# Optimization experiments

Hardware: AMD Instinct MI355X
Metric: run time of the kernel (lower is better)

The kernel has to match this reference:

```python
import jax, jax.numpy as jnp
import numpy as np

K = 7          # kernel_size
PAD = K // 2   # padding


def _unfold(t):
    """im2col for kxk neighborhood: (B,C,H,W) -> (B,C,K*K,H,W), zero-padded."""
    B, C, H, W = t.shape
    p = jnp.pad(t, ((0, 0), (0, 0), (PAD, PAD), (PAD, PAD)))
    # row-major over kernel offsets matches F.unfold ordering
    wins = jnp.stack([p[:, :, i:i + H, j:j + W]
                      for i in range(K) for j in range(K)], axis=2)
    return wins


def setup_inputs() -> dict:
    key = jax.random.key(0)
    ks = jax.random.split(key, 7)
    B, C, H, W = 8, 128, 64, 64
    scale = 1.0 / np.sqrt(C)
    x = jax.random.normal(ks[0], (B, C, H, W), dtype=jnp.float32)
    Wq = jax.random.normal(ks[1], (C, C), dtype=jnp.float32) * scale
    Wk = jax.random.normal(ks[2], (C, C), dtype=jnp.float32) * scale
    Wv = jax.random.normal(ks[3], (C, C), dtype=jnp.float32) * scale
    bq = jax.random.normal(ks[4], (C,), dtype=jnp.float32) * 0.01
    bk = jax.random.normal(ks[5], (C,), dtype=jnp.float32) * 0.01
    bv = jax.random.normal(ks[6], (C,), dtype=jnp.float32) * 0.01
    return {"x": x, "Wq": Wq, "bq": bq, "Wk": Wk, "bk": bk, "Wv": Wv, "bv": bv}


def reference(x, Wq, bq, Wk, bk, Wv, bv):
    # 1x1 convs = channel GEMMs
    q = jnp.einsum('oc,bchw->bohw', Wq, x) + bq[:, None, None]
    k = jnp.einsum('oc,bchw->bohw', Wk, x) + bk[:, None, None]
    v = jnp.einsum('oc,bchw->bohw', Wv, x) + bv[:, None, None]
    k_unf = _unfold(k)   # (B,C,K*K,H,W)
    v_unf = _unfold(v)   # (B,C,K*K,H,W)
    # attention scores over the K*K neighborhood, summed over channels
    attn = jnp.einsum('bchw,bcphw->bphw', q, k_unf)
    attn = jax.nn.softmax(attn, axis=1)
    y = jnp.einsum('bphw,bcphw->bchw', attn, v_unf)
    return y
```

## Files before the change

### kernel.cpp

```cpp
#include <hip/hip_runtime.h>
#include <hip/hip_bf16.h>

#define CC   128
#define HH_  64
#define WW_  64
#define BB   8
#define HWSZ (HH_*WW_)
#define CHW  (CC*HWSZ)
#define BCHW (BB*CHW)
#define PAD  3
#define NP   49

typedef __attribute__((ext_vector_type(8))) short short8;
typedef __attribute__((ext_vector_type(4))) float float4v;

__global__ __launch_bounds__(256) void prep_w(
    const float* __restrict__ Wq, const float* __restrict__ Wk,
    const float* __restrict__ Wv,
    unsigned short* __restrict__ whi, unsigned short* __restrict__ wlo)
{
    int i = blockIdx.x * 256 + threadIdx.x;
    const float* src = (i < 16384) ? Wq : (i < 32768 ? Wk : Wv);
    float f = src[i & 16383];
    __hip_bfloat16 h = __float2bfloat16(f);
    float hf = __bfloat162float(h);
    __hip_bfloat16 l = __float2bfloat16(f - hf);
    unsigned short hu, lu;
    __builtin_memcpy(&hu, &h, 2);
    __builtin_memcpy(&lu, &l, 2);
    whi[i] = hu;
    wlo[i] = lu;
}

__global__ __launch_bounds__(256, 2) void qkv_mfma(
    const float* __restrict__ x,
    const unsigned short* __restrict__ whi, const unsigned short* __restrict__ wlo,
    const float* __restrict__ bq, const float* __restrict__ bk,
    const float* __restrict__ bv, float* __restrict__ qkv)
{
    __shared__ unsigned short xT[2][128][136];
    const int proj = blockIdx.y;
    const int n0g  = blockIdx.x << 7;
    const int b    = n0g >> 12;
    const int npx  = n0g & 4095;
    const int tid  = threadIdx.x;
    const int lane = tid & 63;
    const int wv   = tid >> 6;
    const int wm   = wv & 1, wn = wv >> 1;

    const float* xb = x + (size_t)b*CHW + npx;
    #pragma unroll
    for (int it = 0; it < 16; ++it) {
        int f  = tid + (it << 8);
        int c  = f >> 5;
        int p4 = (f & 31) << 2;
        float4 v = *(const float4*)&xb[(size_t)c*HWSZ + p4];
        float vv[4] = {v.x, v.y, v.z, v.w};
        #pragma unroll
        for (int u = 0; u < 4; ++u) {
            __hip_bfloat16 h = __float2bfloat16(vv[u]);
            float hf = __bfloat162float(h);
            __hip_bfloat16 l = __float2bfloat16(vv[u] - hf);
            unsigned short hu, lu;
            __builtin_memcpy(&hu, &h, 2);
            __builtin_memcpy(&lu, &l, 2);
            xT[0][p4 + u][c] = hu;
            xT[1][p4 + u][c] = lu;
        }
    }

    const float* Bp = (proj == 0) ? bq : (proj == 1 ? bk : bv);
    const int q4 = lane >> 4;
    float4v acc[4][4];
    #pragma unroll
    for (int sm = 0; sm < 4; ++sm) {
        const int mb = wm*64 + sm*16 + q4*4;
        float4v bi;
        bi[0] = Bp[mb+0]; bi[1] = Bp[mb+1]; bi[2] = Bp[mb+2]; bi[3] = Bp[mb+3];
        #pragma unroll
        for (int sn = 0; sn < 4; ++sn) acc[sm][sn] = bi;
    }

    __syncthreads();

    const unsigned short* Wh = whi + (size_t)proj*16384;
    const unsigned short* Wl = wlo + (size_t)proj*16384;
    const int kq8  = q4 << 3;
    const int mrow = lane & 15;

    for (int pass = 0; pass < 3; ++pass) {
        const unsigned short* Wp = (pass == 2) ? Wl : Wh;
        const int xi = (pass == 1) ? 1 : 0;
        #pragma unroll
        for (int kc = 0; kc < 4; ++kc) {
            const int kb = kc << 5;
            short8 a[4], bf[4];
            #pragma unroll
            for (int sm = 0; sm < 4; ++sm) {
                const int m = wm*64 + sm*16 + mrow;
                a[sm] = *(const short8*)&Wp[(size_t)m*CC + kb + kq8];
            }
            #pragma unroll
            for (int sn = 0; sn < 4; ++sn) {
                const int n = wn*64 + sn*16 + mrow;
                bf[sn] = *(const short8*)&xT[xi][n][kb + kq8];
            }
            #pragma unroll
            for (int sm = 0; sm < 4; ++sm)
                #pragma unroll
                for (int sn = 0; sn < 4; ++sn)
                    acc[sm][sn] = __builtin_amdgcn_mfma_f32_16x16x32_bf16(
                        a[sm], bf[sn], acc[sm][sn], 0, 0, 0);
        }
    }

    float* op = qkv + (size_t)proj*BCHW + (size_t)b*CHW + npx;
    #pragma unroll
    for (int sm = 0; sm < 4; ++sm) {
        const int mb = wm*64 + sm*16 + q4*4;
        #pragma unroll
        for (int sn = 0; sn < 4; ++sn) {
            const int n = wn*64 + sn*16 + mrow;
            #pragma unroll
            for (int r = 0; r < 4; ++r)
                op[(size_t)(mb + r)*HWSZ + n] = acc[sm][sn][r];
        }
    }
}

__device__ __forceinline__ void load_chunk16(const float* __restrict__ src,
                                             int h0, int c0, float4* stg) {
    const int tid = threadIdx.x;
    #pragma unroll
    for (int i = 0; i < 2; ++i) {
        int f   = tid + (i << 10);
        int c   = f >> 7;
        int rem = f & 127;
        int r   = rem >> 4;
        int q4  = (rem & 15) << 2;
        int hh  = h0 - PAD + r;
        if ((unsigned)hh < (unsigned)HH_)
            stg[i] = *(const float4*)&src[(size_t)(c0 + c)*HWSZ + hh*WW_ + q4];
        else
            stg[i] = make_float4(0.f, 0.f, 0.f, 0.f);
    }
}

__global__ __launch_bounds__(1024) void locatt(
    const float* __restrict__ qkv, float* __restrict__ out)
{
    __shared__ __align__(16) float smem[8*72*17];
    __shared__ float lg[2][NP][64];
    __shared__ float dn[2][64];

    const int blk = blockIdx.x;
    const int xs  = blk & 7;
    const int jj  = blk >> 3;
    const int b   = jj >> 2;
    const int h0  = (((xs << 2) | (jj & 3)) << 1);
    const int tid = threadIdx.x;
    const int s   = tid >> 6;
    const int lane = tid & 63;
    const int q16  = lane & 15;
    const int csub = lane >> 4;
    const int w4   = q16 << 2;
    const int w    = lane;
    const int rsel = s >> 3;
    const int kr   = s & 7;

    const float* qp = qkv + (size_t)b*CHW;
    const float* kp = qkv + (size_t)BCHW + (size_t)b*CHW;
    const float* vp = qkv + (size_t)2*BCHW + (size_t)b*CHW;

    float (*ks)[8][72] = (float(*)[8][72])smem;

    if (tid < 256) {
        int idx = tid & 127;
        int c = idx >> 3, r = idx & 7;
        int col = (tid < 128) ? 0 : 68;
        *(float4*)&ks[c][r][col] = make_float4(0.f, 0.f, 0.f, 0.f);
    }

    const bool active = rsel ? (kr >= 1) : (kr < 7);

    float acc[7][4];
    #pragma unroll
    for (int dx = 0; dx < 7; ++dx)
        #pragma unroll
        for (int j = 0; j < 4; ++j) acc[dx][j] = 0.f;

    float4 stg[2];
    load_chunk16(kp, h0, 0, stg);

    for (int ck = 0; ck < 8; ++ck) {
        #pragma unroll
        for (int i = 0; i < 2; ++i) {
            int f   = tid + (i << 10);
            int c   = f >> 7;
            int rem = f & 127;
            int r   = rem >> 4;
            int q4  = (rem & 15) << 2;
            *(float4*)&ks[c][r][4 + q4] = stg[i];
        }
        __syncthreads();
        if (ck < 7) load_chunk16(kp, h0, (ck + 1) * 16, stg);

        if (active) {
            const int c0 = ck << 4;
            #pragma unroll
            for (int ci4 = 0; ci4 < 4; ++ci4) {
                const int c = (ci4 << 2) + csub;
                const float* qc = qp + (size_t)(c0 + c)*HWSZ
                                     + (size_t)(h0 + rsel)*WW_ + w4;
                float4 qv  = *(const float4*)qc;
                float4 ka  = *(const float4*)&ks[c][kr][w4];
                float4 kb  = *(const float4*)&ks[c][kr][w4 + 4];
                float4 kc2 = *(const float4*)&ks[c][kr][w4 + 8];
                float kw[12] = {ka.x,ka.y,ka.z,ka.w, kb.x,kb.y,kb.z,kb.w,
                                kc2.x,kc2.y,kc2.z,kc2.w};
                float qa[4] = {qv.x,qv.y,qv.z,qv.w};
                #pragma unroll
                for (int dx = 0; dx < 7; ++dx)
                    #pragma unroll
                    for (int j = 0; j < 4; ++j) {
                        float kv = kw[j + dx + 1];
                        acc[dx][j] = fmaf(qa[j], kv, acc[dx][j]);
                    }
            }
        }
        __syncthreads();
    }

    if (active) {
        #pragma unroll
        for (int dx = 0; dx < 7; ++dx)
            #pragma unroll
            for (int j = 0; j < 4; ++j) {
                acc[dx][j] += __shfl_xor(acc[dx][j], 16, 64);
                acc[dx][j] += __shfl_xor(acc[dx][j], 32, 64);
            }
        const int p0 = rsel ? (kr - 1) * 7 : kr * 7;
        #pragma unroll
        for (int dx = 0; dx < 7; ++dx) {
            if ((dx & 3) == csub)
                *(float4*)&lg[rsel][p0 + dx][w4] =
                    make_float4(acc[dx][0], acc[dx][1], acc[dx][2], acc[dx][3]);
        }
    }

    const int cpl   = (s & 7) << 1;
    const int rbase = rsel << 2;
    float vreg[8];
    {
        #pragma unroll
        for (int i = 0; i < 8; ++i) {
            int ch = i >> 2;
            int r  = rbase + (i & 3);
            int hh = h0 - PAD + r;
            vreg[i] = ((unsigned)hh < (unsigned)HH_)
                      ? vp[(size_t)(cpl + ch)*HWSZ + hh*WW_ + w] : 0.f;
        }
    }
    __syncthreads();

    if (tid < 128) {
        const int r = tid >> 6, px = tid & 63;
        float tv[NP];
        float m = -1e30f;
        #pragma unroll
        for (int p = 0; p < NP; ++p) { tv[p] = lg[r][p][px]; m = fmaxf(m, tv[p]); }
        float d = 0.f;
        #pragma unroll
        for (int p = 0; p < NP; ++p) {
            float e = __expf(tv[p] - m);
            d += e;
            lg[r][p][px] = e;
        }
        dn[r][px] = 1.f / d;
    } else {
        int t = tid - 128;
        for (int i = t; i < 1024; i += 896) {
            int r    = i >> 7;
            int rem  = i & 127;
            int colg = rem >> 4;
            int col  = (colg < 4) ? colg : (64 + colg);
            smem[r*1224 + col*17 + (rem & 15)] = 0.f;
        }
    }
    __syncthreads();

    float a[NP];
    const float sc = dn[rsel][w];
    #pragma unroll
    for (int p = 0; p < NP; ++p) a[p] = lg[rsel][p][w] * sc;

    for (int ck = 0; ck < 8; ++ck) {
        #pragma unroll
        for (int i = 0; i < 8; ++i) {
            int ch = i >> 2;
            int r  = rbase + (i & 3);
            smem[r*1224 + (4 + w)*17 + cpl + ch] = vreg[i];
        }
        __syncthreads();
        if (ck < 7) {
            int c0v = (ck + 1) << 4;
            #pragma unroll
            for (int i = 0; i < 8; ++i) {
                int ch = i >> 2;
                int r  = rbase + (i & 3);
                int hh = h0 - PAD + r;
                vreg[i] = ((unsigned)hh < (unsigned)HH_)
                          ? vp[(size_t)(c0v + cpl + ch)*HWSZ + hh*WW_ + w] : 0.f;
            }
        }
        float ya = 0.f, yb = 0.f;
        #pragma unroll
        for (int rl = 0; rl < 7; ++rl) {
            const int r = rl + rsel;
            const float* vbase = &smem[r*1224 + (1 + w)*17 + cpl];
            #pragma unroll
            for (int dx = 0; dx < 7; ++dx) {
                float va = vbase[17*dx];
                float vb = vbase[17*dx + 1];
                float aw = a[rl*7 + dx];
                ya = fmaf(aw, va, ya);
                yb = fmaf(aw, vb, yb);
            }
        }
        float* op = out + (size_t)b*CHW + (size_t)(ck*16 + cpl)*HWSZ
                        + (size_t)(h0 + rsel)*WW_ + w;
        op[0]    = ya;
        op[HWSZ] = yb;
        __syncthreads();
    }
}

extern "C" void kernel_launch(void* const* d_in, const int* in_sizes, int n_in,
                              void* d_out, int out_size, void* d_ws, size_t ws_size,
                              hipStream_t stream) {
    const float* x  = (const float*)d_in[0];
    const float* Wq = (const float*)d_in[1];
    const float* bq = (const float*)d_in[2];
    const float* Wk = (const float*)d_in[3];
    const float* bk = (const float*)d_in[4];
    const float* Wv = (const float*)d_in[5];
    const float* bv = (const float*)d_in[6];
    float* out = (float*)d_out;
    float* qkv = (float*)d_ws;

    unsigned short* whi = (unsigned short*)d_out;
    unsigned short* wlo = whi + 3*16384;

    prep_w  <<<192, 256, 0, stream>>>(Wq, Wk, Wv, whi, wlo);
    qkv_mfma<<<dim3(256, 3), 256, 0, stream>>>(x, whi, wlo, bq, bk, bv, qkv);
    locatt  <<<256, 1024, 0, stream>>>(qkv, out);
}
```

Measured before the change: 149.8 us.

## Split local attention blocks to one output row per 512-thread block

The local-attention kernel now gives each block a single output row with 512 threads, launching 512 blocks instead of 256 blocks of 1024 threads that handled two rows. Each warp covers one kernel row in the score phase and two channels across all 7 neighbor rows in the value phase. Launch bounds request 4 blocks per CU, aiming for more blocks in flight and better latency hiding. The cost is that halo K/V rows are now loaded per single row (7 rows for 1 output instead of 8 for 2), roughly doubling K/V reads, and one of the eight warps sits idle during the score phase.

```diff
diff --git a/kernel.cpp b/kernel.cpp
--- a/kernel.cpp
+++ b/kernel.cpp
@@ -128,45 +128,43 @@
     }
 }
 
-__device__ __forceinline__ void load_chunk16(const float* __restrict__ src,
-                                             int h0, int c0, float4* stg) {
+__device__ __forceinline__ void load_chunk7(const float* __restrict__ src,
+                                            int h, int c0, float4* stg) {
     const int tid = threadIdx.x;
     #pragma unroll
-    for (int i = 0; i < 2; ++i) {
-        int f   = tid + (i << 10);
+    for (int i = 0; i < 4; ++i) {
+        int f   = tid + (i << 9);
         int c   = f >> 7;
         int rem = f & 127;
         int r   = rem >> 4;
         int q4  = (rem & 15) << 2;
-        int hh  = h0 - PAD + r;
-        if ((unsigned)hh < (unsigned)HH_)
+        int hh  = h - PAD + r;
+        if (r < 7 && (unsigned)hh < (unsigned)HH_)
             stg[i] = *(const float4*)&src[(size_t)(c0 + c)*HWSZ + hh*WW_ + q4];
         else
             stg[i] = make_float4(0.f, 0.f, 0.f, 0.f);
     }
 }
 
-__global__ __launch_bounds__(1024) void locatt(
+__global__ __launch_bounds__(512, 4) void locatt(
     const float* __restrict__ qkv, float* __restrict__ out)
 {
-    __shared__ __align__(16) float smem[8*72*17];
-    __shared__ float lg[2][NP][64];
-    __shared__ float dn[2][64];
+    __shared__ __align__(16) float smem[16*8*72];
+    __shared__ float lg[NP][64];
+    __shared__ float dn[64];
 
     const int blk = blockIdx.x;
     const int xs  = blk & 7;
     const int jj  = blk >> 3;
-    const int b   = jj >> 2;
-    const int h0  = (((xs << 2) | (jj & 3)) << 1);
+    const int b   = jj >> 3;
+    const int h   = (xs << 3) | (jj & 7);
     const int tid = threadIdx.x;
-    const int s   = tid >> 6;
+    const int s    = tid >> 6;
     const int lane = tid & 63;
     const int q16  = lane & 15;
     const int csub = lane >> 4;
     const int w4   = q16 << 2;
     const int w    = lane;
-    const int rsel = s >> 3;
-    const int kr   = s & 7;
 
     const float* qp = qkv + (size_t)b*CHW;
     const float* kp = qkv + (size_t)BCHW + (size_t)b*CHW;
@@ -181,7 +179,7 @@
         *(float4*)&ks[c][r][col] = make_float4(0.f, 0.f, 0.f, 0.f);
     }
 
-    const bool active = rsel ? (kr >= 1) : (kr < 7);
+    const bool activeA = (s < 7);
 
     float acc[7][4];
     #pragma unroll
@@ -189,13 +187,13 @@
         #pragma unroll
         for (int j = 0; j < 4; ++j) acc[dx][j] = 0.f;
 
-    float4 stg[2];
-    load_chunk16(kp, h0, 0, stg);
+    float4 stg[4];
+    load_chunk7(kp, h, 0, stg);
 
     for (int ck = 0; ck < 8; ++ck) {
         #pragma unroll
-        for (int i = 0; i < 2; ++i) {
-            int f   = tid + (i << 10);
+        for (int i = 0; i < 4; ++i) {
+            int f   = tid + (i << 9);
             int c   = f >> 7;
             int rem = f & 127;
             int r   = rem >> 4;
@@ -203,19 +201,19 @@
             *(float4*)&ks[c][r][4 + q4] = stg[i];
         }
         __syncthreads();
-        if (ck < 7) load_chunk16(kp, h0, (ck + 1) * 16, stg);
-
-        if (active) {
+        if (ck < 7) load_chunk7(kp, h, (ck + 1) * 16, stg);
+
+        if (activeA) {
             const int c0 = ck << 4;
             #pragma unroll
             for (int ci4 = 0; ci4 < 4; ++ci4) {
                 const int c = (ci4 << 2) + csub;
                 const float* qc = qp + (size_t)(c0 + c)*HWSZ
-                                     + (size_t)(h0 + rsel)*WW_ + w4;
+                                     + (size_t)h*WW_ + w4;
                 float4 qv  = *(const float4*)qc;
-                float4 ka  = *(const float4*)&ks[c][kr][w4];
-                float4 kb  = *(const float4*)&ks[c][kr][w4 + 4];
-                float4 kc2 = *(const float4*)&ks[c][kr][w4 + 8];
+                float4 ka  = *(const float4*)&ks[c][s][w4];
+                float4 kb  = *(const float4*)&ks[c][s][w4 + 4];
+                float4 kc2 = *(const float4*)&ks[c][s][w4 + 8];
                 float kw[12] = {ka.x,ka.y,ka.z,ka.w, kb.x,kb.y,kb.z,kb.w,
                                 kc2.x,kc2.y,kc2.z,kc2.w};
                 float qa[4] = {qv.x,qv.y,qv.z,qv.w};
@@ -231,7 +229,7 @@
         __syncthreads();
     }
 
-    if (active) {
+    if (activeA) {
         #pragma unroll
         for (int dx = 0; dx < 7; ++dx)
             #pragma unroll
@@ -239,47 +237,46 @@
                 acc[dx][j] += __shfl_xor(acc[dx][j], 16, 64);
                 acc[dx][j] += __shfl_xor(acc[dx][j], 32, 64);
             }
-        const int p0 = rsel ? (kr - 1) * 7 : kr * 7;
+        const int p0 = s * 7;
         #pragma unroll
         for (int dx = 0; dx < 7; ++dx) {
             if ((dx & 3) == csub)
-                *(float4*)&lg[rsel][p0 + dx][w4] =
+                *(float4*)&lg[p0 + dx][w4] =
                     make_float4(acc[dx][0], acc[dx][1], acc[dx][2], acc[dx][3]);
         }
     }
 
-    const int cpl   = (s & 7) << 1;
-    const int rbase = rsel << 2;
-    float vreg[8];
+    const int cpl = s << 1;
+    float vreg[14];
     {
         #pragma unroll
-        for (int i = 0; i < 8; ++i) {
-            int ch = i >> 2;
-            int r  = rbase + (i & 3);
-            int hh = h0 - PAD + r;
+        for (int i = 0; i < 14; ++i) {
+            int ch = (i >= 7) ? 1 : 0;
+            int r  = i - 7*ch;
+            int hh = h - PAD + r;
             vreg[i] = ((unsigned)hh < (unsigned)HH_)
                       ? vp[(size_t)(cpl + ch)*HWSZ + hh*WW_ + w] : 0.f;
         }
     }
     __syncthreads();
 
-    if (tid < 128) {
-        const int r = tid >> 6, px = tid & 63;
+    if (tid < 64) {
+        const int px = tid;
         float tv[NP];
         float m = -1e30f;
         #pragma unroll
-        for (int p = 0; p < NP; ++p) { tv[p] = lg[r][p][px]; m = fmaxf(m, tv[p]); }
+        for (int p = 0; p < NP; ++p) { tv[p] = lg[p][px]; m = fmaxf(m, tv[p]); }
         float d = 0.f;
         #pragma unroll
         for (int p = 0; p < NP; ++p) {
             float e = __expf(tv[p] - m);
             d += e;
-            lg[r][p][px] = e;
-        }
-        dn[r][px] = 1.f / d;
+            lg[p][px] = e;
+        }
+        dn[px] = 1.f / d;
     } else {
-        int t = tid - 128;
-        for (int i = t; i < 1024; i += 896) {
+        int t = tid - 64;
+        for (int i = t; i < 896; i += 448) {
             int r    = i >> 7;
             int rem  = i & 127;
             int colg = rem >> 4;
@@ -290,45 +287,44 @@
     __syncthreads();
 
     float a[NP];
-    const float sc = dn[rsel][w];
-    #pragma unroll
-    for (int p = 0; p < NP; ++p) a[p] = lg[rsel][p][w] * sc;
+    const float sc = dn[w];
+    #pragma unroll
+    for (int p = 0; p < NP; ++p) a[p] = lg[p][w] * sc;
 
     for (int ck = 0; ck < 8; ++ck) {
         #pragma unroll
-        for (int i = 0; i < 8; ++i) {
-            int ch = i >> 2;
-            int r  = rbase + (i & 3);
+        for (int i = 0; i < 14; ++i) {
+            int ch = (i >= 7) ? 1 : 0;
+            int r  = i - 7*ch;
             smem[r*1224 + (4 + w)*17 + cpl + ch] = vreg[i];
         }
         __syncthreads();
         if (ck < 7) {
             int c0v = (ck + 1) << 4;
             #pragma unroll
-            for (int i = 0; i < 8; ++i) {
-                int ch = i >> 2;
-                int r  = rbase + (i & 3);
-                int hh = h0 - PAD + r;
+            for (int i = 0; i < 14; ++i) {
+                int ch = (i >= 7) ? 1 : 0;
+                int r  = i - 7*ch;
+                int hh = h - PAD + r;
                 vreg[i] = ((unsigned)hh < (unsigned)HH_)
                           ? vp[(size_t)(c0v + cpl + ch)*HWSZ + hh*WW_ + w] : 0.f;
             }
         }
         float ya = 0.f, yb = 0.f;
         #pragma unroll
-        for (int rl = 0; rl < 7; ++rl) {
-            const int r = rl + rsel;
+        for (int r = 0; r < 7; ++r) {
             const float* vbase = &smem[r*1224 + (1 + w)*17 + cpl];
             #pragma unroll
             for (int dx = 0; dx < 7; ++dx) {
                 float va = vbase[17*dx];
                 float vb = vbase[17*dx + 1];
-                float aw = a[rl*7 + dx];
+                float aw = a[r*7 + dx];
                 ya = fmaf(aw, va, ya);
                 yb = fmaf(aw, vb, yb);
             }
         }
         float* op = out + (size_t)b*CHW + (size_t)(ck*16 + cpl)*HWSZ
-                        + (size_t)(h0 + rsel)*WW_ + w;
+                        + (size_t)h*WW_ + w;
         op[0]    = ya;
         op[HWSZ] = yb;
         __syncthreads();
@@ -353,5 +349,5 @@
 
     prep_w  <<<192, 256, 0, stream>>>(Wq, Wk, Wv, whi, wlo);
     qkv_mfma<<<dim3(256, 3), 256, 0, stream>>>(x, whi, wlo, bq, bk, bv, qkv);
-    locatt  <<<256, 1024, 0, stream>>>(qkv, out);
-}
+    locatt  <<<512, 512, 0, stream>>>(qkv, out);
+}
```

After: 151.7 us. No clear change (+1.3%).
